# Optimization experiments

Measured on AMD Instinct MI355X. Metric: run time of the kernel, lower is better.

The kernel has to match this reference:

```python
import jax, jax.numpy as jnp
import numpy as np

N = 100000   # nodes
E = 1600000  # edges
D = 128      # input_dim
H = 128      # hidden_dim
G = 64       # graphs in batch
L = 3        # num GCN layers
BN_EPS = 1e-5


def setup_inputs() -> dict:
    key = jax.random.key(0)
    ks = jax.random.split(key, 16)
    s = 1.0 / np.sqrt(H)
    inp = {
        "x": jax.random.normal(ks[0], (N, D), jnp.float32),
        "edge_index": jax.random.randint(ks[1], (2, E), 0, N, dtype=jnp.int64),
        "batch": jnp.sort(jax.random.randint(ks[2], (N,), 0, G, dtype=jnp.int64)),
        # stacked GCNConv params (input_dim == hidden_dim so layer 0 stacks too)
        "conv_w": jax.random.normal(ks[3], (L, H, H), jnp.float32) * s,
        "conv_b": jax.random.normal(ks[4], (L, H), jnp.float32) * 0.01,
        # BatchNorm1d running stats + affine (eval mode)
        "bn_gamma": jnp.ones((L, H), jnp.float32),
        "bn_beta": jnp.zeros((L, H), jnp.float32),
        "bn_mean": jax.random.normal(ks[5], (L, H), jnp.float32) * 0.1,
        "bn_var": jax.random.uniform(ks[6], (L, H), jnp.float32, 0.5, 1.5),
        # node head MLP
        "node_w1": jax.random.normal(ks[7], (H // 2, H), jnp.float32) * s,
        "node_b1": jnp.zeros((H // 2,), jnp.float32),
        "node_w2": jax.random.normal(ks[8], (2, H // 2), jnp.float32) * (1.0 / np.sqrt(H // 2)),
        "node_b2": jnp.zeros((2,), jnp.float32),
        # graph head MLP
        "graph_w1": jax.random.normal(ks[9], (H // 2, H), jnp.float32) * s,
        "graph_b1": jnp.zeros((H // 2,), jnp.float32),
        "graph_w2": jax.random.normal(ks[10], (2, H // 2), jnp.float32) * (1.0 / np.sqrt(H // 2)),
        "graph_b2": jnp.zeros((2,), jnp.float32),
    }
    return inp


def _gcn_layer(h, src, dst, deg_inv_sqrt, w, b):
    # PyG GCNConv: h' = W h, then symmetric-normalized scatter-add over
    # edges (self-loops already appended to src/dst).
    h = h @ w.T                                   # [N, H]
    norm = deg_inv_sqrt[src] * deg_inv_sqrt[dst]  # [E+N]
    msg = h[src] * norm[:, None]                  # [E+N, H] gather
    out = jax.ops.segment_sum(msg, dst, num_segments=N)  # scatter-add
    return out + b


def _forward(x, edge_index, batch, conv_w, conv_b, bn_gamma, bn_beta,
             bn_mean, bn_var, node_w1, node_b1, node_w2, node_b2,
             graph_w1, graph_b1, graph_w2, graph_b2):
    loops = jnp.arange(N, dtype=edge_index.dtype)
    src = jnp.concatenate([edge_index[0], loops])
    dst = jnp.concatenate([edge_index[1], loops])
    deg = jax.ops.segment_sum(jnp.ones_like(src, dtype=x.dtype), dst,
                              num_segments=N)
    deg_inv_sqrt = jnp.where(deg > 0, jax.lax.rsqrt(deg), 0.0)

    h = x
    for i in range(L):  # conv -> BN(eval) -> ReLU (dropout inactive in eval)
        h = _gcn_layer(h, src, dst, deg_inv_sqrt, conv_w[i], conv_b[i])
        h = (h - bn_mean[i]) * jax.lax.rsqrt(bn_var[i] + BN_EPS) * bn_gamma[i] + bn_beta[i]
        h = jax.nn.relu(h)

    node_pred = jax.nn.relu(h @ node_w1.T + node_b1) @ node_w2.T + node_b2

    counts = jax.ops.segment_sum(jnp.ones((N,), h.dtype), batch,
                                 num_segments=G)
    graph_emb = jax.ops.segment_sum(h, batch, num_segments=G) / \
        jnp.maximum(counts, 1.0)[:, None]
    graph_pred = jax.nn.relu(graph_emb @ graph_w1.T + graph_b1) @ graph_w2.T + graph_b2
    return node_pred, graph_pred


def reference(x, edge_index, batch, conv_w, conv_b, bn_gamma, bn_beta,
              bn_mean, bn_var, node_w1, node_b1, node_w2, node_b2,
              graph_w1, graph_b1, graph_w2, graph_b2):
    return _forward(x, edge_index, batch, conv_w, conv_b, bn_gamma, bn_beta,
                    bn_mean, bn_var, node_w1, node_b1, node_w2, node_b2,
                    graph_w1, graph_b1, graph_w2, graph_b2)
```

## Files before the change

kernel.cpp:

```cpp
#include <hip/hip_runtime.h>
#include <hip/hip_bf16.h>

#define NN 100000
#define EE 1600000
#define HH 128
#define GG 64
#define LL 3
#define BN_EPS 1e-5f
#define NT 391
#define CHW 392
#define CAP 6144

typedef __hip_bfloat16 bf16;
typedef __attribute__((ext_vector_type(8))) short short8;
typedef __attribute__((ext_vector_type(4))) float floatx4;

__device__ __forceinline__ float lo16(unsigned v) { return __uint_as_float(v << 16); }
__device__ __forceinline__ float hi16(unsigned v) { return __uint_as_float(v & 0xffff0000u); }
__device__ __forceinline__ unsigned short f2b(float v) {
    bf16 h = __float2bfloat16(v);
    return *(unsigned short*)&h;
}
__device__ __forceinline__ unsigned pack2(float a, float b) {
    return (unsigned)f2b(a) | ((unsigned)f2b(b) << 16);
}
__device__ __forceinline__ int geti(const int* __restrict__ p, int i, int f) {
    return f ? p[2 * i] : p[i];
}

__global__ __launch_bounds__(1024) void k_part(const int* __restrict__ ei,
        unsigned* __restrict__ chunk, unsigned short* __restrict__ lbu,
        int* __restrict__ flag,
        const float* __restrict__ conv_w, const float* __restrict__ nw1,
        unsigned short* __restrict__ cwB, unsigned short* __restrict__ n1B,
        float* __restrict__ bnA, float* __restrict__ bnB,
        const float* __restrict__ conv_b, const float* __restrict__ g,
        const float* __restrict__ be, const float* __restrict__ mn,
        const float* __restrict__ vr, float* __restrict__ gsum,
        float* __restrict__ gcnt) {
    __shared__ int lcnt[NT];
    __shared__ int sd[512];
    __shared__ unsigned short lbs[CHW];
    __shared__ unsigned sorted[4096];
    int t = threadIdx.x;
    int e0 = blockIdx.x * 4096;
    int probe = ei[2 * (e0 + (t & 63)) + 1];
    int f = __any(probe != 0) ? 0 : 1;
    if (blockIdx.x == 0 && t == 0) *flag = f;
    int gi = blockIdx.x * 1024 + t;
    if (gi < LL * HH * HH) cwB[gi] = f2b(conv_w[gi]);
    if (gi < 64 * HH) n1B[gi] = f2b(nw1[gi]);
    if (gi < LL * HH) {
        float A = g[gi] * rsqrtf(vr[gi] + BN_EPS);
        bnA[gi] = A;
        bnB[gi] = (conv_b[gi] - mn[gi]) * A + be[gi];
    }
    if (gi < GG * HH) gsum[gi] = 0.f;
    if (gi < GG) gcnt[gi] = 0.f;
    int nume = EE - e0 < 4096 ? EE - e0 : 4096;
    for (int i = t; i < NT; i += 1024) lcnt[i] = 0;
    __syncthreads();
    unsigned pk[4]; int ml[4], mt[4];
#pragma unroll
    for (int i = 0; i < 4; i++) {
        int li = i * 1024 + t;
        if (li < nume) {
            int e = e0 + li;
            int src = geti(ei, e, f), dst = geti(ei, EE + e, f);
            mt[i] = dst >> 8;
            pk[i] = ((unsigned)src << 8) | (unsigned)(dst & 255);
            ml[i] = atomicAdd(&lcnt[mt[i]], 1);
        }
    }
    __syncthreads();
    int own = 0;
    if (t < 512) {
        own = t < NT ? lcnt[t] : 0;
        sd[t] = own;
    }
    __syncthreads();
    for (int off = 1; off < 512; off <<= 1) {
        int y = 0;
        if (t < 512 && t >= off) y = sd[t - off];
        __syncthreads();
        if (t < 512) sd[t] += y;
        __syncthreads();
    }
    if (t < NT) lbs[t] = (unsigned short)(sd[t] - own);
    if (t == 0) lbs[NT] = (unsigned short)nume;
    __syncthreads();
#pragma unroll
    for (int i = 0; i < 4; i++) {
        int li = i * 1024 + t;
        if (li < nume) sorted[(int)lbs[mt[i]] + ml[i]] = pk[i];
    }
    if (t < CHW) lbu[blockIdx.x * CHW + t] = lbs[t];
    __syncthreads();
    for (int idx = t; idx < nume; idx += 1024)
        __builtin_nontemporal_store(sorted[idx], &chunk[e0 + idx]);
}

__global__ __launch_bounds__(1024) void k_csr(const unsigned* __restrict__ chunk,
        const unsigned short* __restrict__ lbu, unsigned* __restrict__ csr,
        int* __restrict__ offs, int* __restrict__ cnt, float* __restrict__ dinv,
        int* __restrict__ tne) {
    __shared__ unsigned stage[CAP];
    __shared__ unsigned outb[CAP];
    __shared__ int sd[512];
    __shared__ int hist[256], exs[256], cur[256];
    int T = blockIdx.x, t = threadIdx.x;
    int st = 0, rl = 0;
    if (t < NT) {
        int s0 = lbu[t * CHW + T];
        int s1 = lbu[t * CHW + T + 1];
        st = t * 4096 + s0;
        rl = s1 - s0;
    }
    if (t < 512) sd[t] = rl;
    __syncthreads();
    for (int off = 1; off < 512; off <<= 1) {
        int y = 0;
        if (t < 512 && t >= off) y = sd[t - off];
        __syncthreads();
        if (t < 512) sd[t] += y;
        __syncthreads();
    }
    int ne = sd[511];
    if (ne > CAP) ne = CAP;
    int so = t < NT ? sd[t] - rl : 0;
    if (t < 256) hist[t] = 0;
    __syncthreads();
    if (t < NT) {
        for (int j = 0; j < rl; j++) {
            int p = so + j;
            if (p < CAP)
                stage[p] = __builtin_nontemporal_load(&chunk[st + j]);
        }
    }
    __syncthreads();
    for (int i = t; i < ne; i += 1024)
        atomicAdd(&hist[stage[i] & 255u], 1);
    __syncthreads();
    int c = 0;
    if (t < 256) {
        c = hist[t];
        exs[t] = c;
    }
    __syncthreads();
    for (int off = 1; off < 256; off <<= 1) {
        int a = 0;
        if (t < 256 && t >= off) a = exs[t - off];
        __syncthreads();
        if (t < 256) exs[t] += a;
        __syncthreads();
    }
    if (t < 256) {
        int ex = exs[t] - c;
        cur[t] = ex;
        int node = T * 256 + t;
        if (node < NN) {
            offs[node] = T * CAP + ex;
            cnt[node] = c;
            dinv[node] = rsqrtf(1.0f + (float)c);
        }
    }
    if (t == 0) tne[T] = ne;
    __syncthreads();
    for (int i = t; i < ne; i += 1024) {
        unsigned p = stage[i];
        int q = atomicAdd(&cur[p & 255u], 1);
        outb[q] = p >> 8;
    }
    __syncthreads();
    for (int i = t; i < ne; i += 1024)
        csr[(size_t)T * CAP + i] = outb[i];
}

__global__ __launch_bounds__(1024) void k_wpack(const unsigned* __restrict__ csr,
        const float* __restrict__ dinv, unsigned* __restrict__ ewp,
        const int* __restrict__ tne) {
    int T = blockIdx.x, t = threadIdx.x;
    int ne = tne[T];
    for (int i = t; i < ne; i += 1024) {
        unsigned s = csr[(size_t)T * CAP + i];
        ewp[(size_t)T * CAP + i] = (s << 15) | ((unsigned)f2b(dinv[s]) & 0x7fffu);
    }
}

template<typename AT, int NC, bool FUSE>
__global__ __launch_bounds__(256) void k_gemm(const AT* __restrict__ in,
        const unsigned short* __restrict__ Wb, const float* __restrict__ bias,
        unsigned short* __restrict__ outh, int do_relu,
        const float* __restrict__ w2, const float* __restrict__ b2v,
        float* __restrict__ out2f) {
    int wave = threadIdx.x >> 6, lane = threadIdx.x & 63;
    int ln = lane & 15, q = lane >> 4;
    int r0 = blockIdx.x * 64 + wave * 16;
    int row = r0 + ln;
    int rr = row < NN ? row : NN - 1;
    short8 a[4];
    if constexpr (sizeof(AT) == 2) {
        const short8* ap = (const short8*)(in + (size_t)rr * HH);
#pragma unroll
        for (int kt = 0; kt < 4; kt++) a[kt] = ap[kt * 4 + q];
    } else {
        const float4* ap = (const float4*)(in + (size_t)rr * HH);
#pragma unroll
        for (int kt = 0; kt < 4; kt++) {
            float4 f0 = ap[(kt * 4 + q) * 2];
            float4 f1 = ap[(kt * 4 + q) * 2 + 1];
            a[kt][0] = (short)f2b(f0.x); a[kt][1] = (short)f2b(f0.y);
            a[kt][2] = (short)f2b(f0.z); a[kt][3] = (short)f2b(f0.w);
            a[kt][4] = (short)f2b(f1.x); a[kt][5] = (short)f2b(f1.y);
            a[kt][6] = (short)f2b(f1.z); a[kt][7] = (short)f2b(f1.w);
        }
    }
    float p0[4], p1[4];
    if constexpr (FUSE) {
#pragma unroll
        for (int r = 0; r < 4; r++) { p0[r] = 0.f; p1[r] = 0.f; }
    }
#pragma unroll
    for (int ct = 0; ct < NC / 16; ct++) {
        int c = ct * 16 + ln;
        const short8* bp = (const short8*)(Wb + (size_t)c * HH);
        floatx4 acc = {0.f, 0.f, 0.f, 0.f};
#pragma unroll
        for (int kt = 0; kt < 4; kt++) {
            short8 b = bp[kt * 4 + q];
            acc = __builtin_amdgcn_mfma_f32_16x16x32_bf16(a[kt], b, acc, 0, 0, 0);
        }
        float bv = bias ? bias[c] : 0.f;
        if constexpr (FUSE) {
            float wa = w2[c], wb = w2[64 + c];
#pragma unroll
            for (int reg = 0; reg < 4; reg++) {
                float v = fmaxf(acc[reg] + bv, 0.f);
                p0[reg] = fmaf(v, wa, p0[reg]);
                p1[reg] = fmaf(v, wb, p1[reg]);
            }
        } else {
#pragma unroll
            for (int reg = 0; reg < 4; reg++) {
                int orow = r0 + q * 4 + reg;
                if (orow < NN) {
                    float v = acc[reg] + bv;
                    if (do_relu) v = fmaxf(v, 0.f);
                    outh[(size_t)orow * NC + c] = f2b(v);
                }
            }
        }
    }
    if constexpr (FUSE) {
#pragma unroll
        for (int off = 1; off < 16; off <<= 1) {
#pragma unroll
            for (int r = 0; r < 4; r++) {
                p0[r] += __shfl_xor(p0[r], off);
                p1[r] += __shfl_xor(p1[r], off);
            }
        }
        if (ln == 0) {
            float ba = b2v[0], bb = b2v[1];
#pragma unroll
            for (int reg = 0; reg < 4; reg++) {
                int orow = r0 + q * 4 + reg;
                if (orow < NN)
                    ((float2*)out2f)[orow] = make_float2(p0[reg] + ba, p1[reg] + bb);
            }
        }
    }
}

__global__ __launch_bounds__(256) void k_aggr(const uint2* __restrict__ tH2,
        const unsigned* __restrict__ ewp, const int* __restrict__ offs,
        const int* __restrict__ cnt, const float* __restrict__ dinv,
        const float* __restrict__ bnA, const float* __restrict__ bnB,
        uint2* __restrict__ hout) {
    int wave = threadIdx.x >> 6, lane = threadIdx.x & 63;
    int node = blockIdx.x * 4 + wave;
    if (node >= NN) return;
    int base = offs[node], ne = cnt[node];
    float dd = dinv[node];
    int half = lane >> 5, li = lane & 31;
    uint2 sv = tH2[(size_t)node * 32 + li];
    float ws = half ? 0.f : dd;
    float4 acc;
    acc.x = lo16(sv.x) * ws; acc.y = hi16(sv.x) * ws;
    acc.z = lo16(sv.y) * ws; acc.w = hi16(sv.y) * ws;
    for (int k0 = 0; k0 < ne; k0 += 64) {
        int idx = k0 + lane;
        unsigned m = idx < ne ? __builtin_nontemporal_load(&ewp[base + idx]) : 0u;
        int c2 = ne - k0 < 64 ? ne - k0 : 64;
        for (int kk = 0; kk < c2; kk += 16) {
            uint2 vv[8]; float wj[8];
#pragma unroll
            for (int j = 0; j < 8; j++) {
                int e = kk + 2 * j + half;
                unsigned mm = (unsigned)__shfl((int)m, e);
                int s = (int)(mm >> 15);
                wj[j] = __uint_as_float((mm & 0x7fffu) << 16);
                vv[j] = tH2[(size_t)s * 32 + li];
            }
#pragma unroll
            for (int j = 0; j < 8; j++) {
                acc.x = fmaf(lo16(vv[j].x), wj[j], acc.x);
                acc.y = fmaf(hi16(vv[j].x), wj[j], acc.y);
                acc.z = fmaf(lo16(vv[j].y), wj[j], acc.z);
                acc.w = fmaf(hi16(vv[j].y), wj[j], acc.w);
            }
        }
    }
    acc.x += __shfl_xor(acc.x, 32);
    acc.y += __shfl_xor(acc.y, 32);
    acc.z += __shfl_xor(acc.z, 32);
    acc.w += __shfl_xor(acc.w, 32);
    if (half == 0) {
        float4 Av = ((const float4*)bnA)[li];
        float4 Bv = ((const float4*)bnB)[li];
        float r0 = fmaxf(fmaf(acc.x * dd, Av.x, Bv.x), 0.f);
        float r1 = fmaxf(fmaf(acc.y * dd, Av.y, Bv.y), 0.f);
        float r2 = fmaxf(fmaf(acc.z * dd, Av.z, Bv.z), 0.f);
        float r3 = fmaxf(fmaf(acc.w * dd, Av.w, Bv.w), 0.f);
        unsigned long long v64 =
            ((unsigned long long)pack2(r2, r3) << 32) | pack2(r0, r1);
        __builtin_nontemporal_store(v64,
            (unsigned long long*)&hout[(size_t)node * 32 + li]);
    }
}

#define PN 32
__global__ __launch_bounds__(64) void k_pool(const unsigned* __restrict__ hb,
        const int* __restrict__ batch, float* __restrict__ gsum,
        float* __restrict__ gcnt, const int* __restrict__ flag) {
    int lane = threadIdx.x;
    int f = *flag;
    int s0 = blockIdx.x * PN;
    int e0 = s0 + PN < NN ? s0 + PN : NN;
    int cur = geti(batch, s0, f);
    float a0 = 0.f, a1 = 0.f, cn = 0.f;
    for (int n = s0; n < e0; n++) {
        int g = geti(batch, n, f);
        if (g != cur) {
            atomicAdd(&gsum[cur * HH + 2 * lane], a0);
            atomicAdd(&gsum[cur * HH + 2 * lane + 1], a1);
            if (lane == 0) atomicAdd(&gcnt[cur], cn);
            a0 = a1 = cn = 0.f; cur = g;
        }
        unsigned v = hb[(size_t)n * 64 + lane];
        a0 += lo16(v); a1 += hi16(v); cn += 1.f;
    }
    atomicAdd(&gsum[cur * HH + 2 * lane], a0);
    atomicAdd(&gsum[cur * HH + 2 * lane + 1], a1);
    if (lane == 0) atomicAdd(&gcnt[cur], cn);
}

__global__ __launch_bounds__(64) void k_ghead(const float* __restrict__ gsum,
        const float* __restrict__ gcnt, const float* __restrict__ w1,
        const float* __restrict__ b1, const float* __restrict__ w2,
        const float* __restrict__ b2v, float* __restrict__ out) {
    __shared__ float emb[HH];
    int g = blockIdx.x, lane = threadIdx.x;
    float cn = gcnt[g];
    cn = cn > 1.f ? cn : 1.f;
    float inv = 1.f / cn;
    emb[lane] = gsum[g * HH + lane] * inv;
    emb[lane + 64] = gsum[g * HH + 64 + lane] * inv;
    __syncthreads();
    float acc = b1[lane];
    for (int k = 0; k < HH; k++) acc = fmaf(emb[k], w1[lane * HH + k], acc);
    float y = fmaxf(acc, 0.f);
    float v0 = y * w2[lane];
    float v1 = y * w2[64 + lane];
#pragma unroll
    for (int off = 32; off; off >>= 1) {
        v0 += __shfl_xor(v0, off);
        v1 += __shfl_xor(v1, off);
    }
    if (lane == 0) {
        out[(size_t)NN * 2 + g * 2]     = v0 + b2v[0];
        out[(size_t)NN * 2 + g * 2 + 1] = v1 + b2v[1];
    }
}

extern "C" void kernel_launch(void* const* d_in, const int* in_sizes, int n_in,
                              void* d_out, int out_size, void* d_ws, size_t ws_size,
                              hipStream_t stream) {
    const float* x      = (const float*)d_in[0];
    const int*   ei     = (const int*)d_in[1];
    const int*   batch  = (const int*)d_in[2];
    const float* conv_w = (const float*)d_in[3];
    const float* conv_b = (const float*)d_in[4];
    const float* bn_g   = (const float*)d_in[5];
    const float* bn_b   = (const float*)d_in[6];
    const float* bn_m   = (const float*)d_in[7];
    const float* bn_v   = (const float*)d_in[8];
    const float* nw1    = (const float*)d_in[9];
    const float* nb1    = (const float*)d_in[10];
    const float* nw2    = (const float*)d_in[11];
    const float* nb2    = (const float*)d_in[12];
    const float* gw1    = (const float*)d_in[13];
    const float* gb1    = (const float*)d_in[14];
    const float* gw2    = (const float*)d_in[15];
    const float* gb2    = (const float*)d_in[16];
    float* out = (float*)d_out;

    char* ws = (char*)d_ws;
    size_t off = 0;
    auto alloc = [&](size_t bytes) -> void* {
        void* p = ws + off;
        off += (bytes + 255) & ~(size_t)255;
        return p;
    };
    unsigned short* hb   = (unsigned short*)alloc((size_t)NN * HH * 2);
    unsigned short* tb   = (unsigned short*)alloc((size_t)NN * HH * 2);
    unsigned* chunk  = (unsigned*)alloc((size_t)EE * 4);
    unsigned* csr    = (unsigned*)alloc((size_t)NT * CAP * 4);
    unsigned* ewp    = (unsigned*)alloc((size_t)NT * CAP * 4);
    unsigned short* lbu = (unsigned short*)alloc((size_t)NT * CHW * 2);
    int*      offs   = (int*)     alloc((size_t)NN * 4);
    int*      cnt    = (int*)     alloc((size_t)NN * 4);
    float*    dinv   = (float*)   alloc((size_t)NN * 4);
    int*      tne    = (int*)     alloc((size_t)NT * 4);
    float*    bnA    = (float*)   alloc((size_t)LL * HH * 4);
    float*    bnB    = (float*)   alloc((size_t)LL * HH * 4);
    float*    gsum   = (float*)   alloc((size_t)GG * HH * 4);
    float*    gcnt   = (float*)   alloc((size_t)GG * 4);
    unsigned short* cwB = (unsigned short*)alloc((size_t)LL * HH * HH * 2);
    unsigned short* n1B = (unsigned short*)alloc((size_t)64 * HH * 2);
    int*      flag   = (int*)     alloc(256);

    k_part<<<NT, 1024, 0, stream>>>(ei, chunk, lbu, flag, conv_w, nw1, cwB, n1B,
            bnA, bnB, conv_b, bn_g, bn_b, bn_m, bn_v, gsum, gcnt);
    k_csr<<<NT, 1024, 0, stream>>>(chunk, lbu, csr, offs, cnt, dinv, tne);
    k_wpack<<<NT, 1024, 0, stream>>>(csr, dinv, ewp, tne);

    k_gemm<float, HH, false><<<(NN + 63) / 64, 256, 0, stream>>>(
        x, cwB, nullptr, tb, 0, nullptr, nullptr, nullptr);
    k_aggr<<<(NN + 3) / 4, 256, 0, stream>>>((const uint2*)tb, ewp, offs, cnt,
                                             dinv, bnA, bnB, (uint2*)hb);
    for (int l = 1; l < LL; l++) {
        k_gemm<unsigned short, HH, false><<<(NN + 63) / 64, 256, 0, stream>>>(
            hb, cwB + (size_t)l * HH * HH, nullptr, tb, 0, nullptr, nullptr, nullptr);
        k_aggr<<<(NN + 3) / 4, 256, 0, stream>>>((const uint2*)tb, ewp, offs, cnt,
                                                 dinv, bnA + l * HH, bnB + l * HH,
                                                 (uint2*)hb);
    }

    k_gemm<unsigned short, 64, true><<<(NN + 63) / 64, 256, 0, stream>>>(
        hb, n1B, nb1, nullptr, 1, nw2, nb2, out);

    k_pool<<<(NN + PN - 1) / PN, 64, 0, stream>>>((const unsigned*)hb, batch,
                                                  gsum, gcnt, flag);
    k_ghead<<<GG, 64, 0, stream>>>(gsum, gcnt, gw1, gb1, gw2, gb2, out);
}
```

Measured before the change: 505.1 us.

## Sort CSR by source sub-bins, stage GEMM weights in LDS, deepen gather and pool loads

The CSR build now sorts each destination's edges by the high bits of the source index, using a 2048-bin histogram and a 1024-wide scan, so neighbor gathers walk memory in a more local order. The GEMM kernel copies its weight matrix into padded LDS once per block instead of reading it from global memory per wave. The aggregation loop processes 16 gathered rows per batch instead of 8, putting more loads in flight at the cost of more registers. The pooling loop is unrolled by 4 and drops the end-of-range bound, which is only safe because N is a multiple of 32.

```diff
diff --git a/kernel.cpp b/kernel.cpp
--- a/kernel.cpp
+++ b/kernel.cpp
@@ -10,6 +10,7 @@
 #define NT 391
 #define CHW 392
 #define CAP 6144
+#define NBIN 2048
 
 typedef __hip_bfloat16 bf16;
 typedef __attribute__((ext_vector_type(8))) short short8;
@@ -106,8 +107,8 @@
         int* __restrict__ tne) {
     __shared__ unsigned stage[CAP];
     __shared__ unsigned outb[CAP];
-    __shared__ int sd[512];
-    __shared__ int hist[256], exs[256], cur[256];
+    __shared__ int sd[1024];
+    __shared__ int hist[NBIN], cur[NBIN];
     int T = blockIdx.x, t = threadIdx.x;
     int st = 0, rl = 0;
     if (t < NT) {
@@ -128,7 +129,7 @@
     int ne = sd[511];
     if (ne > CAP) ne = CAP;
     int so = t < NT ? sd[t] - rl : 0;
-    if (t < 256) hist[t] = 0;
+    for (int i = t; i < NBIN; i += 1024) hist[i] = 0;
     __syncthreads();
     if (t < NT) {
         for (int j = 0; j < rl; j++) {
@@ -138,28 +139,33 @@
         }
     }
     __syncthreads();
-    for (int i = t; i < ne; i += 1024)
-        atomicAdd(&hist[stage[i] & 255u], 1);
-    __syncthreads();
-    int c = 0;
+    for (int i = t; i < ne; i += 1024) {
+        unsigned p = stage[i];
+        int bin = (int)((p & 255u) << 3) | (int)((p >> 8) >> 14);
+        atomicAdd(&hist[bin], 1);
+    }
+    __syncthreads();
+    int v0 = hist[2 * t], v1 = hist[2 * t + 1];
+    int sp = v0 + v1;
+    sd[t] = sp;
+    __syncthreads();
+    for (int off = 1; off < 1024; off <<= 1) {
+        int y = t >= off ? sd[t - off] : 0;
+        __syncthreads();
+        sd[t] += y;
+        __syncthreads();
+    }
+    int base = sd[t] - sp;
+    cur[2 * t] = base;
+    cur[2 * t + 1] = base + v0;
+    __syncthreads();
     if (t < 256) {
-        c = hist[t];
-        exs[t] = c;
-    }
-    __syncthreads();
-    for (int off = 1; off < 256; off <<= 1) {
-        int a = 0;
-        if (t < 256 && t >= off) a = exs[t - off];
-        __syncthreads();
-        if (t < 256) exs[t] += a;
-        __syncthreads();
-    }
-    if (t < 256) {
-        int ex = exs[t] - c;
-        cur[t] = ex;
+        int stn = cur[t * 8];
+        int nxt = t == 255 ? ne : cur[(t + 1) * 8];
+        int c = nxt - stn;
         int node = T * 256 + t;
         if (node < NN) {
-            offs[node] = T * CAP + ex;
+            offs[node] = T * CAP + stn;
             cnt[node] = c;
             dinv[node] = rsqrtf(1.0f + (float)c);
         }
@@ -168,7 +174,8 @@
     __syncthreads();
     for (int i = t; i < ne; i += 1024) {
         unsigned p = stage[i];
-        int q = atomicAdd(&cur[p & 255u], 1);
+        int bin = (int)((p & 255u) << 3) | (int)((p >> 8) >> 14);
+        int q = atomicAdd(&cur[bin], 1);
         outb[q] = p >> 8;
     }
     __syncthreads();
@@ -193,8 +200,16 @@
         unsigned short* __restrict__ outh, int do_relu,
         const float* __restrict__ w2, const float* __restrict__ b2v,
         float* __restrict__ out2f) {
+    __shared__ char sB[NC * 272];
     int wave = threadIdx.x >> 6, lane = threadIdx.x & 63;
     int ln = lane & 15, q = lane >> 4;
+    {
+        const short8* wsrc = (const short8*)Wb;
+        for (int i = threadIdx.x; i < NC * 16; i += 256) {
+            short8 v = wsrc[i];
+            *(short8*)(sB + (i >> 4) * 272 + (i & 15) * 16) = v;
+        }
+    }
     int r0 = blockIdx.x * 64 + wave * 16;
     int row = r0 + ln;
     int rr = row < NN ? row : NN - 1;
@@ -215,6 +230,7 @@
             a[kt][6] = (short)f2b(f1.z); a[kt][7] = (short)f2b(f1.w);
         }
     }
+    __syncthreads();
     float p0[4], p1[4];
     if constexpr (FUSE) {
 #pragma unroll
@@ -223,11 +239,10 @@
 #pragma unroll
     for (int ct = 0; ct < NC / 16; ct++) {
         int c = ct * 16 + ln;
-        const short8* bp = (const short8*)(Wb + (size_t)c * HH);
         floatx4 acc = {0.f, 0.f, 0.f, 0.f};
 #pragma unroll
         for (int kt = 0; kt < 4; kt++) {
-            short8 b = bp[kt * 4 + q];
+            short8 b = *(const short8*)(sB + (size_t)c * 272 + kt * 64 + q * 16);
             acc = __builtin_amdgcn_mfma_f32_16x16x32_bf16(a[kt], b, acc, 0, 0, 0);
         }
         float bv = bias ? bias[c] : 0.f;
@@ -292,10 +307,10 @@
         int idx = k0 + lane;
         unsigned m = idx < ne ? __builtin_nontemporal_load(&ewp[base + idx]) : 0u;
         int c2 = ne - k0 < 64 ? ne - k0 : 64;
-        for (int kk = 0; kk < c2; kk += 16) {
-            uint2 vv[8]; float wj[8];
-#pragma unroll
-            for (int j = 0; j < 8; j++) {
+        for (int kk = 0; kk < c2; kk += 32) {
+            uint2 vv[16]; float wj[16];
+#pragma unroll
+            for (int j = 0; j < 16; j++) {
                 int e = kk + 2 * j + half;
                 unsigned mm = (unsigned)__shfl((int)m, e);
                 int s = (int)(mm >> 15);
@@ -303,7 +318,7 @@
                 vv[j] = tH2[(size_t)s * 32 + li];
             }
 #pragma unroll
-            for (int j = 0; j < 8; j++) {
+            for (int j = 0; j < 16; j++) {
                 acc.x = fmaf(lo16(vv[j].x), wj[j], acc.x);
                 acc.y = fmaf(hi16(vv[j].x), wj[j], acc.y);
                 acc.z = fmaf(lo16(vv[j].y), wj[j], acc.z);
@@ -336,19 +351,25 @@
     int lane = threadIdx.x;
     int f = *flag;
     int s0 = blockIdx.x * PN;
-    int e0 = s0 + PN < NN ? s0 + PN : NN;
     int cur = geti(batch, s0, f);
     float a0 = 0.f, a1 = 0.f, cn = 0.f;
-    for (int n = s0; n < e0; n++) {
-        int g = geti(batch, n, f);
+    auto step = [&](int g, unsigned v) {
         if (g != cur) {
             atomicAdd(&gsum[cur * HH + 2 * lane], a0);
             atomicAdd(&gsum[cur * HH + 2 * lane + 1], a1);
             if (lane == 0) atomicAdd(&gcnt[cur], cn);
             a0 = a1 = cn = 0.f; cur = g;
         }
-        unsigned v = hb[(size_t)n * 64 + lane];
         a0 += lo16(v); a1 += hi16(v); cn += 1.f;
+    };
+    for (int n = s0; n < s0 + PN; n += 4) {
+        int g0 = geti(batch, n, f),     g1 = geti(batch, n + 1, f);
+        int g2 = geti(batch, n + 2, f), g3 = geti(batch, n + 3, f);
+        unsigned v0 = hb[(size_t)n * 64 + lane];
+        unsigned v1 = hb[(size_t)(n + 1) * 64 + lane];
+        unsigned v2 = hb[(size_t)(n + 2) * 64 + lane];
+        unsigned v3 = hb[(size_t)(n + 3) * 64 + lane];
+        step(g0, v0); step(g1, v1); step(g2, v2); step(g3, v3);
     }
     atomicAdd(&gsum[cur * HH + 2 * lane], a0);
     atomicAdd(&gsum[cur * HH + 2 * lane + 1], a1);
```

After: 485.6 us. 1.04x faster.
